# Optimization experiments

Hardware: AMD Instinct MI355X
Metric: run time of the kernel (lower is better)

Reference implementation:

```python
import jax, jax.numpy as jnp
import numpy as np

MESSAGE_PASSES = 3  # constants.message_passes
F_NODE = 64   # hidden_node_features
F_EDGE = 16   # n_edge_features
M_MSG = 64    # message_size
OUT_DIM = 128
B, N = 8, 256
EDGE_DENSITY = 0.1


def setup_inputs() -> dict:
    key = jax.random.key(0)
    ks = jax.random.split(key, 12)
    nodes = jax.random.normal(ks[0], (B, N, F_NODE), dtype=jnp.float32)
    # sparse positive edge features: rand * bernoulli connectivity (avg degree ~ N*density)
    raw = jax.random.uniform(ks[1], (B, N, N, F_EDGE), dtype=jnp.float32)
    conn = (jax.random.uniform(ks[2], (B, N, N)) < EDGE_DENSITY).astype(jnp.float32)
    edges = raw * conn[..., None]
    s = 0.05
    return {
        "nodes": nodes,
        "edges": edges,
        # message MLP: cat(neighbour, edge) -> message_size
        "W_msg": jax.random.normal(ks[3], (F_NODE + F_EDGE, M_MSG), dtype=jnp.float32) * s,
        "b_msg": jnp.zeros((M_MSG,), dtype=jnp.float32),
        # GRU cell (input=message_size, hidden=F_NODE), gates [r|z|n]
        "W_i": jax.random.normal(ks[4], (M_MSG, 3 * F_NODE), dtype=jnp.float32) * s,
        "W_h": jax.random.normal(ks[5], (F_NODE, 3 * F_NODE), dtype=jnp.float32) * s,
        "b_i": jnp.zeros((3 * F_NODE,), dtype=jnp.float32),
        "b_h": jnp.zeros((3 * F_NODE,), dtype=jnp.float32),
        # gated readout
        "W_g": jax.random.normal(ks[6], (2 * F_NODE, OUT_DIM), dtype=jnp.float32) * s,
        "b_g": jnp.zeros((OUT_DIM,), dtype=jnp.float32),
        "W_e": jax.random.normal(ks[7], (F_NODE, OUT_DIM), dtype=jnp.float32) * s,
        "b_e": jnp.zeros((OUT_DIM,), dtype=jnp.float32),
    }


def reference(nodes, edges, W_msg, b_msg, W_i, W_h, b_i, b_h, W_g, b_g, W_e, b_e):
    # adjacency[b,i,j] != 0  <=>  edge (i<-j) exists (original: edges.sum(3).nonzero)
    adjacency = edges.sum(axis=-1)                                   # (B,N,N)
    nbr_mask = (adjacency != 0).astype(nodes.dtype)                  # (B,N,N)
    node_mask = (adjacency.sum(axis=-1) != 0)                        # (B,N) bool
    node_mask_f = node_mask.astype(nodes.dtype)

    h = nodes                                                        # hidden_nodes init = nodes
    b, n, f = nodes.shape
    for _ in range(MESSAGE_PASSES):
        # message_terms over all (node i, neighbour j) pairs; masked sum == padded-gather sum
        nghb = jnp.broadcast_to(h[:, None, :, :], (b, n, n, f))      # (B,N,N,F) neighbour feats
        feat = jnp.concatenate([nghb, edges], axis=-1)               # (B,N,N,F+E)
        terms = jax.nn.relu(feat @ W_msg + b_msg)                    # (B,N,N,M)
        messages = jnp.einsum('bijm,bij->bim', terms, nbr_mask)      # summation aggregation
        # GRU cell update
        gi = messages @ W_i + b_i                                    # (B,N,3F)
        gh = h @ W_h + b_h
        ir, iz, inn = jnp.split(gi, 3, axis=-1)
        hr, hz, hn = jnp.split(gh, 3, axis=-1)
        r = jax.nn.sigmoid(ir + hr)
        z = jax.nn.sigmoid(iz + hz)
        ng = jnp.tanh(inn + r * hn)
        h_new = (1.0 - z) * ng + z * h
        # only nodes with nonzero degree are scattered back (original indexes node_batch idc)
        h = jnp.where(node_mask[..., None], h_new, h)

    # gated readout: sum_i mask_i * sigmoid(g([h_i, x_i])) * e(h_i)
    gate = jax.nn.sigmoid(jnp.concatenate([h, nodes], axis=-1) @ W_g + b_g)  # (B,N,OUT)
    emb = h @ W_e + b_e                                                      # (B,N,OUT)
    out = jnp.einsum('bno,bn->bo', gate * emb, node_mask_f)                  # (B,OUT)
    return out
```

## Files before the change

### kernel.cpp

```cpp
#include <hip/hip_runtime.h>
#include <hip/hip_bf16.h>

#define BB 8
#define NN 256
#define FF 64
#define EE 16
#define MM 64
#define G3 192
#define OUTD 128
#define ROWS (BB*NN)
#define MAXD 64
#define RPB 4

__device__ __forceinline__ float sigmoidf_(float x) {
    return 1.0f / (1.0f + __expf(-x));
}

__global__ __launch_bounds__(256) void k_prep(
    const float* __restrict__ nodes, const float* __restrict__ edges,
    const float* __restrict__ Wmsg, const float* __restrict__ bmsg,
    int* __restrict__ deg, int* __restrict__ nbr,
    float* __restrict__ h, float* __restrict__ hn, float* __restrict__ out)
{
    int row = blockIdx.x;
    int tid = threadIdx.x;
    int lane = tid & 63, wv = tid >> 6;
    __shared__ int wcnt[4];
    __shared__ float snode[FF];

    const float4* ep = (const float4*)(edges + (((size_t)row) * NN + tid) * EE);
    float4 a = ep[0], b4 = ep[1], c4 = ep[2], d4 = ep[3];
    float s = a.x+a.y+a.z+a.w + b4.x+b4.y+b4.z+b4.w
            + c4.x+c4.y+c4.z+c4.w + d4.x+d4.y+d4.z+d4.w;
    bool pred = (s != 0.0f);
    unsigned long long m = __ballot(pred);
    if (lane == 0) wcnt[wv] = __popcll(m);
    if (tid < FF) snode[tid] = nodes[(size_t)row * FF + tid];
    __syncthreads();

    int base = 0;
    #pragma unroll
    for (int q = 0; q < 4; ++q) base += (q < wv) ? wcnt[q] : 0;
    int slot = base + __popcll(m & ((1ull << lane) - 1ull));
    if (pred && slot < MAXD) nbr[row * MAXD + slot] = tid;

    if (tid == 0) {
        int tot = wcnt[0] + wcnt[1] + wcnt[2] + wcnt[3];
        deg[row] = (tot < MAXD) ? tot : MAXD;
    }
    if (tid < FF) h[row * FF + tid] = snode[tid];
    if (tid < MM) {
        float acc = bmsg[tid];
        #pragma unroll 8
        for (int k = 0; k < FF; ++k) acc += snode[k] * Wmsg[k * MM + tid];
        hn[row * MM + tid] = acc;
    }
    if (row == 0) {
        #pragma unroll
        for (int i = 0; i < (BB * OUTD) / 256; ++i) out[i * 256 + tid] = 0.0f;
    }
}

__global__ __launch_bounds__(512, 8) void k_pass4(
    const float* __restrict__ edges,
    const float* __restrict__ Wmsg, const float* __restrict__ bmsg,
    const float* __restrict__ Wi, const float* __restrict__ Wh,
    const float* __restrict__ bi, const float* __restrict__ bh,
    const float* __restrict__ nodes,
    const float* __restrict__ Wg, const float* __restrict__ bg,
    const float* __restrict__ We, const float* __restrict__ be,
    const int* __restrict__ deg, const int* __restrict__ nbr,
    const float* __restrict__ hn_in, float* __restrict__ hn_out,
    float* __restrict__ h, float* __restrict__ out, int last)
{
    const int r0   = blockIdx.x * RPB;
    const int b    = r0 >> 8;
    const int tid  = threadIdx.x;
    const int w    = tid >> 6;
    const int lane = tid & 63;

    __shared__ int   snbr[RPB][MAXD];
    __shared__ int   sdeg[RPB];
    __shared__ float efeat[RPB][MAXD][EE];
    __shared__ float part[8][MM];
    __shared__ float smsg[RPB][MM];
    __shared__ float sh[RPB][FF];
    __shared__ float sx[RPB][FF];
    __shared__ float pg[6][RPB][FF];
    __shared__ float sg[RPB][OUTD];
    __shared__ float se[RPB][OUTD];

    if (tid < RPB) sdeg[tid] = deg[r0 + tid];
    if (tid < RPB * MAXD) {
        snbr[tid >> 6][tid & 63] = nbr[(r0 + (tid >> 6)) * MAXD + (tid & 63)];
        if (last) {
            int r = tid >> 6, k = tid & 63;
            sx[r][k] = nodes[(size_t)(r0 + r) * FF + k];
        }
    } else {
        int x = tid - RPB * MAXD;
        sh[x >> 6][x & 63] = h[(size_t)(r0 + (x >> 6)) * FF + (x & 63)];
    }

    float we[EE];
    #pragma unroll
    for (int k = 0; k < EE; ++k) we[k] = Wmsg[(FF + k) * MM + lane];
    __syncthreads();

    #pragma unroll
    for (int r = 0; r < RPB; ++r) {
        int cnt4 = sdeg[r] * 4;
        for (int i = tid; i < cnt4; i += 512) {
            int slot = i >> 2, q = i & 3;
            const float4* src =
                (const float4*)(edges + (((size_t)(r0 + r)) * NN + snbr[r][slot]) * EE);
            ((float4*)&efeat[r][slot][0])[q] = src[q];
        }
    }
    __syncthreads();

    {
        int r = w >> 1, sub = w & 1;
        int d = sdeg[r];
        const float* hb = hn_in + (size_t)b * NN * MM;
        float acc = 0.0f;
        for (int s = sub; s < d; s += 2) {
            int j = snbr[r][s];
            float term = hb[j * MM + lane];
            #pragma unroll
            for (int k = 0; k < EE; ++k) term += efeat[r][s][k] * we[k];
            acc += fmaxf(term, 0.0f);
        }
        part[w][lane] = acc;
    }
    __syncthreads();
    if (tid < RPB * MM) {
        int r = tid >> 6, tt = tid & 63;
        smsg[r][tt] = part[2*r][tt] + part[2*r+1][tt];
    }
    __syncthreads();

    if (w < 3) {
        float a0 = bi[w * FF + lane], a1 = a0, a2 = a0, a3 = a0;
        #pragma unroll 4
        for (int k = 0; k < FF; ++k) {
            float wgt = Wi[k * G3 + w * FF + lane];
            a0 += smsg[0][k] * wgt; a1 += smsg[1][k] * wgt;
            a2 += smsg[2][k] * wgt; a3 += smsg[3][k] * wgt;
        }
        pg[w][0][lane] = a0; pg[w][1][lane] = a1;
        pg[w][2][lane] = a2; pg[w][3][lane] = a3;
    } else if (w < 6) {
        int g = w - 3;
        float a0 = bh[g * FF + lane], a1 = a0, a2 = a0, a3 = a0;
        #pragma unroll 4
        for (int k = 0; k < FF; ++k) {
            float wgt = Wh[k * G3 + g * FF + lane];
            a0 += sh[0][k] * wgt; a1 += sh[1][k] * wgt;
            a2 += sh[2][k] * wgt; a3 += sh[3][k] * wgt;
        }
        pg[3 + g][0][lane] = a0; pg[3 + g][1][lane] = a1;
        pg[3 + g][2][lane] = a2; pg[3 + g][3][lane] = a3;
    }
    __syncthreads();

    if (tid < RPB * FF) {
        int r = tid >> 6, tt = tid & 63;
        float rr = sigmoidf_(pg[0][r][tt] + pg[3][r][tt]);
        float zz = sigmoidf_(pg[1][r][tt] + pg[4][r][tt]);
        float ng = tanhf(pg[2][r][tt] + rr * pg[5][r][tt]);
        float hold = sh[r][tt];
        float hnew = (1.0f - zz) * ng + zz * hold;
        if (sdeg[r] == 0) hnew = hold;
        sh[r][tt] = hnew;
        if (!last) h[(size_t)(r0 + r) * FF + tt] = hnew;
    }
    __syncthreads();

    if (!last) {
        {
            int r = w >> 1, kh = w & 1;
            float p = 0.0f;
            #pragma unroll
            for (int kk = 0; kk < 32; ++kk) {
                int k = kh * 32 + kk;
                p += sh[r][k] * Wmsg[k * MM + lane];
            }
            part[w][lane] = p;
        }
        __syncthreads();
        if (tid < RPB * MM) {
            int r = tid >> 6, tt = tid & 63;
            hn_out[(size_t)(r0 + r) * MM + tt] = bmsg[tt]
                + part[2*r][tt] + part[2*r+1][tt];
        }
    } else {
        int r = tid >> 7, o = tid & 127;
        float g = bg[o], e = be[o];
        #pragma unroll 4
        for (int k = 0; k < FF; ++k) {
            float hk = sh[r][k];
            g += hk * Wg[k * OUTD + o];
            e += hk * We[k * OUTD + o];
        }
        #pragma unroll 4
        for (int k = 0; k < FF; ++k) g += sx[r][k] * Wg[(FF + k) * OUTD + o];
        sg[r][o] = g; se[r][o] = e;
        __syncthreads();
        if (tid < OUTD) {
            float v = 0.0f;
            #pragma unroll
            for (int r2 = 0; r2 < RPB; ++r2)
                v += (sdeg[r2] != 0) ? sigmoidf_(sg[r2][tid]) * se[r2][tid] : 0.0f;
            atomicAdd(&out[b * OUTD + tid], v);
        }
    }
}

extern "C" void kernel_launch(void* const* d_in, const int* in_sizes, int n_in,
                              void* d_out, int out_size, void* d_ws, size_t ws_size,
                              hipStream_t stream) {
    const float* nodes = (const float*)d_in[0];
    const float* edges = (const float*)d_in[1];
    const float* Wmsg  = (const float*)d_in[2];
    const float* bmsg  = (const float*)d_in[3];
    const float* Wi    = (const float*)d_in[4];
    const float* Wh    = (const float*)d_in[5];
    const float* bi    = (const float*)d_in[6];
    const float* bh    = (const float*)d_in[7];
    const float* Wg    = (const float*)d_in[8];
    const float* bg    = (const float*)d_in[9];
    const float* We    = (const float*)d_in[10];
    const float* be    = (const float*)d_in[11];
    float* out = (float*)d_out;
    char* ws = (char*)d_ws;

    int*   deg  = (int*)ws;
    int*   nbr  = (int*)(ws + 8192);
    float* h    = (float*)(ws + 8192 + (size_t)ROWS * MAXD * 4);
    float* hnA  = h   + (size_t)ROWS * FF;
    float* hnB  = hnA + (size_t)ROWS * MM;

    k_prep<<<ROWS, 256, 0, stream>>>(nodes, edges, Wmsg, bmsg, deg, nbr, h, hnA, out);

    k_pass4<<<ROWS/RPB, 512, 0, stream>>>(edges, Wmsg, bmsg, Wi, Wh, bi, bh,
                                          nodes, Wg, bg, We, be, deg, nbr,
                                          hnA, hnB, h, out, 0);
    k_pass4<<<ROWS/RPB, 512, 0, stream>>>(edges, Wmsg, bmsg, Wi, Wh, bi, bh,
                                          nodes, Wg, bg, We, be, deg, nbr,
                                          hnB, hnA, h, out, 0);
    k_pass4<<<ROWS/RPB, 512, 0, stream>>>(edges, Wmsg, bmsg, Wi, Wh, bi, bh,
                                          nodes, Wg, bg, We, be, deg, nbr,
                                          hnA, hnB, h, out, 1);
}
```

Before: 151.3 us.

## Double block size to 1024 threads and split per-row work across more warps

Grows the pass kernel from 512 to 1024 threads per block. The neighbour aggregation now uses four waves per row instead of two. The GRU gate matvecs split K into two halves across twelve waves, and the readout splits gate and embedding across separate thread groups. The aim is to cut the serial per-wave work in each phase and raise latency hiding, at the cost of more barriers, larger shared partial buffers and possibly lower occupancy from the 1024-thread blocks.

```diff
diff --git a/kernel.cpp b/kernel.cpp
--- a/kernel.cpp
+++ b/kernel.cpp
@@ -61,7 +61,7 @@
     }
 }
 
-__global__ __launch_bounds__(512, 8) void k_pass4(
+__global__ __launch_bounds__(1024, 8) void k_pass4(
     const float* __restrict__ edges,
     const float* __restrict__ Wmsg, const float* __restrict__ bmsg,
     const float* __restrict__ Wi, const float* __restrict__ Wh,
@@ -82,24 +82,23 @@
     __shared__ int   snbr[RPB][MAXD];
     __shared__ int   sdeg[RPB];
     __shared__ float efeat[RPB][MAXD][EE];
-    __shared__ float part[8][MM];
+    __shared__ float part[16][MM];
     __shared__ float smsg[RPB][MM];
     __shared__ float sh[RPB][FF];
     __shared__ float sx[RPB][FF];
-    __shared__ float pg[6][RPB][FF];
+    __shared__ float pg[6][2][RPB][FF];
     __shared__ float sg[RPB][OUTD];
     __shared__ float se[RPB][OUTD];
 
     if (tid < RPB) sdeg[tid] = deg[r0 + tid];
     if (tid < RPB * MAXD) {
         snbr[tid >> 6][tid & 63] = nbr[(r0 + (tid >> 6)) * MAXD + (tid & 63)];
-        if (last) {
-            int r = tid >> 6, k = tid & 63;
-            sx[r][k] = nodes[(size_t)(r0 + r) * FF + k];
-        }
-    } else {
+    } else if (tid < 2 * RPB * MAXD) {
         int x = tid - RPB * MAXD;
         sh[x >> 6][x & 63] = h[(size_t)(r0 + (x >> 6)) * FF + (x & 63)];
+    } else if (last && tid < 3 * RPB * MAXD) {
+        int x = tid - 2 * RPB * MAXD;
+        sx[x >> 6][x & 63] = nodes[(size_t)(r0 + (x >> 6)) * FF + (x & 63)];
     }
 
     float we[EE];
@@ -110,7 +109,7 @@
     #pragma unroll
     for (int r = 0; r < RPB; ++r) {
         int cnt4 = sdeg[r] * 4;
-        for (int i = tid; i < cnt4; i += 512) {
+        for (int i = tid; i < cnt4; i += 1024) {
             int slot = i >> 2, q = i & 3;
             const float4* src =
                 (const float4*)(edges + (((size_t)(r0 + r)) * NN + snbr[r][slot]) * EE);
@@ -120,11 +119,11 @@
     __syncthreads();
 
     {
-        int r = w >> 1, sub = w & 1;
+        int r = w >> 2, sub = w & 3;
         int d = sdeg[r];
         const float* hb = hn_in + (size_t)b * NN * MM;
         float acc = 0.0f;
-        for (int s = sub; s < d; s += 2) {
+        for (int s = sub; s < d; s += 4) {
             int j = snbr[r][s];
             float term = hb[j * MM + lane];
             #pragma unroll
@@ -136,39 +135,43 @@
     __syncthreads();
     if (tid < RPB * MM) {
         int r = tid >> 6, tt = tid & 63;
-        smsg[r][tt] = part[2*r][tt] + part[2*r+1][tt];
-    }
-    __syncthreads();
-
-    if (w < 3) {
-        float a0 = bi[w * FF + lane], a1 = a0, a2 = a0, a3 = a0;
-        #pragma unroll 4
-        for (int k = 0; k < FF; ++k) {
-            float wgt = Wi[k * G3 + w * FF + lane];
-            a0 += smsg[0][k] * wgt; a1 += smsg[1][k] * wgt;
-            a2 += smsg[2][k] * wgt; a3 += smsg[3][k] * wgt;
-        }
-        pg[w][0][lane] = a0; pg[w][1][lane] = a1;
-        pg[w][2][lane] = a2; pg[w][3][lane] = a3;
-    } else if (w < 6) {
-        int g = w - 3;
-        float a0 = bh[g * FF + lane], a1 = a0, a2 = a0, a3 = a0;
-        #pragma unroll 4
-        for (int k = 0; k < FF; ++k) {
-            float wgt = Wh[k * G3 + g * FF + lane];
-            a0 += sh[0][k] * wgt; a1 += sh[1][k] * wgt;
-            a2 += sh[2][k] * wgt; a3 += sh[3][k] * wgt;
-        }
-        pg[3 + g][0][lane] = a0; pg[3 + g][1][lane] = a1;
-        pg[3 + g][2][lane] = a2; pg[3 + g][3][lane] = a3;
+        smsg[r][tt] = part[4*r][tt] + part[4*r+1][tt] + part[4*r+2][tt] + part[4*r+3][tt];
+    }
+    __syncthreads();
+
+    if (w < 12) {
+        int g = w >> 1, kh = w & 1;
+        float a0 = 0, a1 = 0, a2 = 0, a3 = 0;
+        if (g < 3) {
+            for (int k = kh * 32; k < kh * 32 + 32; ++k) {
+                float wgt = Wi[k * G3 + g * FF + lane];
+                a0 += smsg[0][k] * wgt; a1 += smsg[1][k] * wgt;
+                a2 += smsg[2][k] * wgt; a3 += smsg[3][k] * wgt;
+            }
+        } else {
+            int gg = g - 3;
+            for (int k = kh * 32; k < kh * 32 + 32; ++k) {
+                float wgt = Wh[k * G3 + gg * FF + lane];
+                a0 += sh[0][k] * wgt; a1 += sh[1][k] * wgt;
+                a2 += sh[2][k] * wgt; a3 += sh[3][k] * wgt;
+            }
+        }
+        pg[g][kh][0][lane] = a0; pg[g][kh][1][lane] = a1;
+        pg[g][kh][2][lane] = a2; pg[g][kh][3][lane] = a3;
     }
     __syncthreads();
 
     if (tid < RPB * FF) {
         int r = tid >> 6, tt = tid & 63;
-        float rr = sigmoidf_(pg[0][r][tt] + pg[3][r][tt]);
-        float zz = sigmoidf_(pg[1][r][tt] + pg[4][r][tt]);
-        float ng = tanhf(pg[2][r][tt] + rr * pg[5][r][tt]);
+        float ir  = bi[tt]        + pg[0][0][r][tt] + pg[0][1][r][tt];
+        float iz  = bi[FF + tt]   + pg[1][0][r][tt] + pg[1][1][r][tt];
+        float in_ = bi[2*FF + tt] + pg[2][0][r][tt] + pg[2][1][r][tt];
+        float hr  = bh[tt]        + pg[3][0][r][tt] + pg[3][1][r][tt];
+        float hz  = bh[FF + tt]   + pg[4][0][r][tt] + pg[4][1][r][tt];
+        float hnn = bh[2*FF + tt] + pg[5][0][r][tt] + pg[5][1][r][tt];
+        float rr = sigmoidf_(ir + hr);
+        float zz = sigmoidf_(iz + hz);
+        float ng = tanhf(in_ + rr * hnn);
         float hold = sh[r][tt];
         float hnew = (1.0f - zz) * ng + zz * hold;
         if (sdeg[r] == 0) hnew = hold;
@@ -178,7 +181,7 @@
     __syncthreads();
 
     if (!last) {
-        {
+        if (w < 8) {
             int r = w >> 1, kh = w & 1;
             float p = 0.0f;
             #pragma unroll
@@ -195,17 +198,21 @@
                 + part[2*r][tt] + part[2*r+1][tt];
         }
     } else {
-        int r = tid >> 7, o = tid & 127;
-        float g = bg[o], e = be[o];
-        #pragma unroll 4
-        for (int k = 0; k < FF; ++k) {
-            float hk = sh[r][k];
-            g += hk * Wg[k * OUTD + o];
-            e += hk * We[k * OUTD + o];
-        }
-        #pragma unroll 4
-        for (int k = 0; k < FF; ++k) g += sx[r][k] * Wg[(FF + k) * OUTD + o];
-        sg[r][o] = g; se[r][o] = e;
+        int grp = tid >> 7, o = tid & 127;
+        int r = grp >> 1, kind = grp & 1;
+        if (kind == 0) {
+            float g = bg[o];
+            #pragma unroll 4
+            for (int k = 0; k < FF; ++k) g += sh[r][k] * Wg[k * OUTD + o];
+            #pragma unroll 4
+            for (int k = 0; k < FF; ++k) g += sx[r][k] * Wg[(FF + k) * OUTD + o];
+            sg[r][o] = g;
+        } else {
+            float e = be[o];
+            #pragma unroll 4
+            for (int k = 0; k < FF; ++k) e += sh[r][k] * We[k * OUTD + o];
+            se[r][o] = e;
+        }
         __syncthreads();
         if (tid < OUTD) {
             float v = 0.0f;
@@ -243,13 +250,13 @@
 
     k_prep<<<ROWS, 256, 0, stream>>>(nodes, edges, Wmsg, bmsg, deg, nbr, h, hnA, out);
 
-    k_pass4<<<ROWS/RPB, 512, 0, stream>>>(edges, Wmsg, bmsg, Wi, Wh, bi, bh,
-                                          nodes, Wg, bg, We, be, deg, nbr,
-                                          hnA, hnB, h, out, 0);
-    k_pass4<<<ROWS/RPB, 512, 0, stream>>>(edges, Wmsg, bmsg, Wi, Wh, bi, bh,
-                                          nodes, Wg, bg, We, be, deg, nbr,
-                                          hnB, hnA, h, out, 0);
-    k_pass4<<<ROWS/RPB, 512, 0, stream>>>(edges, Wmsg, bmsg, Wi, Wh, bi, bh,
-                                          nodes, Wg, bg, We, be, deg, nbr,
-                                          hnA, hnB, h, out, 1);
-}
+    k_pass4<<<ROWS/RPB, 1024, 0, stream>>>(edges, Wmsg, bmsg, Wi, Wh, bi, bh,
+                                           nodes, Wg, bg, We, be, deg, nbr,
+                                           hnA, hnB, h, out, 0);
+    k_pass4<<<ROWS/RPB, 1024, 0, stream>>>(edges, Wmsg, bmsg, Wi, Wh, bi, bh,
+                                           nodes, Wg, bg, We, be, deg, nbr,
+                                           hnB, hnA, h, out, 0);
+    k_pass4<<<ROWS/RPB, 1024, 0, stream>>>(edges, Wmsg, bmsg, Wi, Wh, bi, bh,
+                                           nodes, Wg, bg, We, be, deg, nbr,
+                                           hnA, hnB, h, out, 1);
+}
```

New measurement: 146.5 us. 1.03x faster.
